# Kernel tuning notes

Hardware: AMD Instinct MI355X
Metric: run time of the kernel (lower is better)

## Reference

```python
import jax, jax.numpy as jnp
import numpy as np

N_NODES = 100000
N_EDGES = 1600000
D_FEAT = 128
HIDDEN = 128
N_CLASSES = 10
N_GRAPHS = 64


def setup_inputs() -> dict:
    key = jax.random.key(0)
    ks = jax.random.split(key, 8)
    x = jax.random.normal(ks[0], (N_NODES, D_FEAT), dtype=jnp.float32)
    edge_index = jax.random.randint(ks[1], (2, N_EDGES), 0, N_NODES, dtype=jnp.int64)
    batch = jnp.sort(jax.random.randint(ks[2], (N_NODES,), 0, N_GRAPHS, dtype=jnp.int64))
    # GraphConv params: lin_rel (weight+bias) applied to aggregated neighbors,
    # lin_root (weight only) applied to self features. Final classifier lin.
    s = 1.0 / np.sqrt(D_FEAT)
    w_rel = jax.random.uniform(ks[3], (HIDDEN, D_FEAT), jnp.float32, -s, s)
    b_rel = jax.random.uniform(ks[4], (HIDDEN,), jnp.float32, -s, s)
    w_root = jax.random.uniform(ks[5], (HIDDEN, D_FEAT), jnp.float32, -s, s)
    sl = 1.0 / np.sqrt(HIDDEN)
    w_lin = jax.random.uniform(ks[6], (N_CLASSES, HIDDEN), jnp.float32, -sl, sl)
    b_lin = jax.random.uniform(ks[7], (N_CLASSES,), jnp.float32, -sl, sl)
    return {"x": x, "edge_index": edge_index, "batch": batch,
            "w_rel": w_rel, "b_rel": b_rel, "w_root": w_root,
            "w_lin": w_lin, "b_lin": b_lin}


def reference(x, edge_index, batch, w_rel, b_rel, w_root, w_lin, b_lin):
    src, dst = edge_index[0], edge_index[1]
    # GraphConv(aggr='add'): gather source features, scatter-add to targets
    agg = jax.ops.segment_sum(x[src], dst, num_segments=N_NODES)  # [N, F]
    h = agg @ w_rel.T + b_rel + x @ w_root.T                      # [N, H]
    # global_mean_pool over graph ids
    summed = jax.ops.segment_sum(h, batch, num_segments=N_GRAPHS)            # [G, H]
    counts = jax.ops.segment_sum(jnp.ones((N_NODES,), h.dtype), batch,
                                 num_segments=N_GRAPHS)                       # [G]
    pooled = summed / jnp.maximum(counts, 1.0)[:, None]
    # final classifier (dropout==0 so it is a no-op)
    return pooled @ w_lin.T + b_lin                                # [G, C]
```

## Files before the change

kernel.cpp:

```cpp
#include <hip/hip_runtime.h>

#define N_NODES  100000
#define N_EDGES  1600000
#define D        128
#define NG       64
#define NC       10
#define NBMAX    512
#define TILE     64
#define EPT      8
#define ABLK     196
#define NBUCK    391
#define BCAP     8192
#define CBLK2    98
#define CIW      68
#define XSW      130

typedef unsigned int uint;
typedef unsigned short ushort;
typedef unsigned long long ull;
typedef short bhalf8 __attribute__((ext_vector_type(8)));
typedef float f32x4  __attribute__((ext_vector_type(4)));

#define MFMA_BF16 __builtin_amdgcn_mfma_f32_16x16x32_bf16

#define OFF_COUNTS 391
#define ZERO_U32   512
#define BDATA_U32  (NBUCK * (BCAP / 2))

static_assert(ABLK * 1024 * EPT >= N_EDGES, "edge coverage");
static_assert(NBUCK * 256 >= N_NODES, "bucket coverage");

__global__ __launch_bounds__(256) void fill_kernel(uint* __restrict__ p)
{
    const int i = blockIdx.x * 256 + threadIdx.x;
    if (i < ZERO_U32) p[i] = 0u;
}

__global__ __launch_bounds__(1024) void bucket_kernel(
    const int* __restrict__ ei, const int* __restrict__ batch,
    uint* __restrict__ tail, int* __restrict__ counts,
    ushort* __restrict__ bdata)
{
    const int b = blockIdx.x;
    if (b < ABLK) {
        __shared__ uint hs[NBUCK];
        __shared__ uint he[NBUCK];
        const int t = threadIdx.x;
        for (int i = t; i < NBUCK; i += 1024) hs[i] = 0u;
        __syncthreads();

        const int e0 = b * (1024 * EPT) + t * EPT;
        uint er[EPT];
        int  s[EPT], dn[EPT];
        bool v[EPT];
        if (e0 + EPT <= N_EDGES) {
            const int4 a0 = *reinterpret_cast<const int4*>(ei + e0);
            const int4 a1 = *reinterpret_cast<const int4*>(ei + e0 + 4);
            const int4 b0 = *reinterpret_cast<const int4*>(ei + N_EDGES + e0);
            const int4 b1 = *reinterpret_cast<const int4*>(ei + N_EDGES + e0 + 4);
            s[0]=a0.x; s[1]=a0.y; s[2]=a0.z; s[3]=a0.w;
            s[4]=a1.x; s[5]=a1.y; s[6]=a1.z; s[7]=a1.w;
            dn[0]=b0.x; dn[1]=b0.y; dn[2]=b0.z; dn[3]=b0.w;
            dn[4]=b1.x; dn[5]=b1.y; dn[6]=b1.z; dn[7]=b1.w;
            #pragma unroll
            for (int i = 0; i < EPT; ++i) v[i] = true;
        } else {
            #pragma unroll
            for (int i = 0; i < EPT; ++i) {
                v[i] = (e0 + i) < N_EDGES;
                s[i]  = v[i] ? ei[e0 + i] : 0;
                dn[i] = v[i] ? ei[N_EDGES + e0 + i] : 0;
            }
        }
        #pragma unroll
        for (int i = 0; i < EPT; ++i) {
            if (v[i]) {
                const uint g = (uint)batch[dn[i]];
                const uint k = (uint)s[i] >> 8;
                er[i] = (k << 16) | (((uint)s[i] & 255u) << 6) | g;
                atomicAdd(&hs[k], 1u);
            } else er[i] = 0xFFFFFFFFu;
        }
        __syncthreads();
        if (t < NBUCK) {
            const uint c = hs[t];
            uint r = 0u, a = 0u;
            if (c) { a = (c + 31u) & ~31u; r = atomicAdd(&tail[t], a); }
            hs[t] = r;
            he[t] = r + a;
        }
        __syncthreads();
        #pragma unroll
        for (int i = 0; i < EPT; ++i) {
            if (er[i] != 0xFFFFFFFFu) {
                const uint k = er[i] >> 16;
                const uint pos = atomicAdd(&hs[k], 1u);
                if (pos < BCAP)
                    bdata[(size_t)k * BCAP + pos] = (ushort)(er[i] & 0xFFFFu);
            }
        }
        __syncthreads();
        if (t < NBUCK) {
            uint p = hs[t];
            uint e = he[t];
            if (e > BCAP) e = BCAP;
            for (; p < e; ++p) bdata[(size_t)t * BCAP + p] = 0xFFFFu;
        }
    } else {
        const int n = (b - ABLK) * 1024 + threadIdx.x;
        if (n >= N_NODES) return;
        const int lane = threadIdx.x & 63;
        const int g = batch[n];
        const bool lead = (n == 0) || (lane == 0) || (batch[n - 1] != g);
        const ull bl = __ballot(lead);
        if (lead) {
            const ull higher = (lane == 63) ? 0ull : (bl >> (lane + 1));
            int end = higher ? (lane + 1 + (__ffsll(higher) - 1)) : 64;
            const int wb = n - lane;
            int nv = N_NODES - wb; if (nv > 64) nv = 64;
            if (end > nv) end = nv;
            atomicAdd(&counts[g], end - lane);
        }
    }
}

__device__ __forceinline__ uint packbf(float f)
{
    const uint u  = __float_as_uint(f);
    const uint hb = (u + 0x7FFFu + ((u >> 16) & 1u)) >> 16;
    const float hf = __uint_as_float(hb << 16);
    const uint ul = __float_as_uint(f - hf);
    const uint lb = (ul + 0x7FFFu + ((ul >> 16) & 1u)) >> 16;
    return hb | (lb << 16);
}

__global__ __launch_bounds__(1024, 8) void gemm_kernel(
    const float* __restrict__ x,
    const uint* __restrict__ tail, const ushort* __restrict__ bdata,
    const int* __restrict__ batch,
    float* __restrict__ partA, float* __restrict__ partX, int NBe)
{
    __shared__ uint xsp[TILE * XSW];
    __shared__ uint ci[NG * CIW];
    __shared__ uint h[TILE * NG];

    const int t   = threadIdx.x;
    const int l   = t & 63;
    const int w   = t >> 6;
    const int mt  = w & 3;
    const int nt0 = (w >> 2) << 1;
    const int lr  = l & 15;
    const int lh  = l >> 4;

    f32x4 aA0 = {0,0,0,0}, aA1 = {0,0,0,0};
    f32x4 aX0 = {0,0,0,0}, aX1 = {0,0,0,0};

    const int ntiles = (N_NODES + TILE - 1) / TILE;
    for (int tb = blockIdx.x; tb < ntiles; tb += NBe) {
        const int base   = tb * TILE;
        const int nvalid = min(TILE, N_NODES - base);
        const int bk     = tb >> 2;
        const uint qsel  = (uint)(tb & 3);

        #pragma unroll
        for (int k = 0; k < 4; ++k) h[t + k * 1024] = 0u;
        #pragma unroll
        for (int k = 0; k < 2; ++k) {
            const int f4i = t + k * 1024;
            const int n = f4i >> 5, c4 = f4i & 31;
            float4 v = make_float4(0.f, 0.f, 0.f, 0.f);
            if (n < nvalid)
                v = *reinterpret_cast<const float4*>(x + (size_t)(base + n) * D + c4 * 4);
            uint2 p01, p23;
            p01.x = packbf(v.x); p01.y = packbf(v.y);
            p23.x = packbf(v.z); p23.y = packbf(v.w);
            uint* dst = xsp + n * XSW + c4 * 4;
            *reinterpret_cast<uint2*>(dst)     = p01;
            *reinterpret_cast<uint2*>(dst + 2) = p23;
        }
        __syncthreads();

        {
            uint nrec = tail[bk]; if (nrec > BCAP) nrec = BCAP;
            const ushort* __restrict__ bp = bdata + (size_t)bk * BCAP;
            for (uint i = (uint)t; i < nrec; i += 1024u) {
                const uint r = bp[i];
                if (r != 0xFFFFu && ((r >> 12) & 3u) == qsel)
                    atomicAdd(&h[((r >> 6) & 63u) * NG + (r & 63u)], 1u);
            }
        }
        __syncthreads();

        {
            const int node = t >> 4, slot = t & 15;
            const int gb = (node < nvalid) ? batch[base + node] : -1;
            const uint4 hv = *reinterpret_cast<const uint4*>(&h[node * NG + slot * 4]);
            const uint hc[4] = {hv.x, hv.y, hv.z, hv.w};
            #pragma unroll
            for (int j = 0; j < 4; ++j) {
                const int g = slot * 4 + j;
                uint val = __float_as_uint((float)hc[j]) >> 16;
                if (gb == g) val |= 0x3F800000u;
                ci[g * CIW + node] = val;
            }
        }
        __syncthreads();

        #pragma unroll
        for (int kc = 0; kc < 2; ++kc) {
            const int k0 = kc * 32;
            const uint* cip = ci + (mt * 16 + lr) * CIW + k0 + lh * 8;
            const uint4 ca = *reinterpret_cast<const uint4*>(cip);
            const uint4 cb = *reinterpret_cast<const uint4*>(cip + 4);
            bhalf8 acnt, aind;
            acnt[0]=(short)ca.x; aind[0]=(short)(ca.x>>16);
            acnt[1]=(short)ca.y; aind[1]=(short)(ca.y>>16);
            acnt[2]=(short)ca.z; aind[2]=(short)(ca.z>>16);
            acnt[3]=(short)ca.w; aind[3]=(short)(ca.w>>16);
            acnt[4]=(short)cb.x; aind[4]=(short)(cb.x>>16);
            acnt[5]=(short)cb.y; aind[5]=(short)(cb.y>>16);
            acnt[6]=(short)cb.z; aind[6]=(short)(cb.z>>16);
            acnt[7]=(short)cb.w; aind[7]=(short)(cb.w>>16);

            const uint* xb = xsp + (k0 + lh * 8) * XSW + lr;
            {
                const uint* xp = xb + nt0 * 16;
                const uint r0=xp[0],      r1=xp[XSW],   r2=xp[2*XSW], r3=xp[3*XSW],
                           r4=xp[4*XSW],  r5=xp[5*XSW], r6=xp[6*XSW], r7=xp[7*XSW];
                bhalf8 bh, bl;
                bh[0]=(short)r0; bl[0]=(short)(r0>>16);
                bh[1]=(short)r1; bl[1]=(short)(r1>>16);
                bh[2]=(short)r2; bl[2]=(short)(r2>>16);
                bh[3]=(short)r3; bl[3]=(short)(r3>>16);
                bh[4]=(short)r4; bl[4]=(short)(r4>>16);
                bh[5]=(short)r5; bl[5]=(short)(r5>>16);
                bh[6]=(short)r6; bl[6]=(short)(r6>>16);
                bh[7]=(short)r7; bl[7]=(short)(r7>>16);
                aA0 = MFMA_BF16(acnt, bh, aA0, 0, 0, 0);
                aA0 = MFMA_BF16(acnt, bl, aA0, 0, 0, 0);
                aX0 = MFMA_BF16(aind, bh, aX0, 0, 0, 0);
                aX0 = MFMA_BF16(aind, bl, aX0, 0, 0, 0);
            }
            {
                const uint* xp = xb + (nt0 + 1) * 16;
                const uint r0=xp[0],      r1=xp[XSW],   r2=xp[2*XSW], r3=xp[3*XSW],
                           r4=xp[4*XSW],  r5=xp[5*XSW], r6=xp[6*XSW], r7=xp[7*XSW];
                bhalf8 bh, bl;
                bh[0]=(short)r0; bl[0]=(short)(r0>>16);
                bh[1]=(short)r1; bl[1]=(short)(r1>>16);
                bh[2]=(short)r2; bl[2]=(short)(r2>>16);
                bh[3]=(short)r3; bl[3]=(short)(r3>>16);
                bh[4]=(short)r4; bl[4]=(short)(r4>>16);
                bh[5]=(short)r5; bl[5]=(short)(r5>>16);
                bh[6]=(short)r6; bl[6]=(short)(r6>>16);
                bh[7]=(short)r7; bl[7]=(short)(r7>>16);
                aA1 = MFMA_BF16(acnt, bh, aA1, 0, 0, 0);
                aA1 = MFMA_BF16(acnt, bl, aA1, 0, 0, 0);
                aX1 = MFMA_BF16(aind, bh, aX1, 0, 0, 0);
                aX1 = MFMA_BF16(aind, bl, aX1, 0, 0, 0);
            }
        }
        __syncthreads();
    }

    float* pa = partA + (size_t)blockIdx.x * (NG * D);
    float* px = partX + (size_t)blockIdx.x * (NG * D);
    #pragma unroll
    for (int r = 0; r < 4; ++r) {
        const int row = mt * 16 + lh * 4 + r;
        pa[row * D + nt0 * 16 + lr]       = aA0[r];
        pa[row * D + (nt0 + 1) * 16 + lr] = aA1[r];
        px[row * D + nt0 * 16 + lr]       = aX0[r];
        px[row * D + (nt0 + 1) * 16 + lr] = aX1[r];
    }
}

__global__ __launch_bounds__(256) void reduce1_kernel(
    const float* __restrict__ partA, const float* __restrict__ partX,
    float* __restrict__ tmp2, int NBe)
{
    const int cb = blockIdx.x & 63;
    const int pc = blockIdx.x >> 6;
    const int c  = cb * 256 + threadIdx.x;
    const float* __restrict__ srcp =
        (c < NG * D) ? (partA + c) : (partX + (c - NG * D));
    const int chunk = (NBe + 3) >> 2;
    const int p0 = pc * chunk;
    int p1 = p0 + chunk; if (p1 > NBe) p1 = NBe;
    float s = 0.f;
    #pragma unroll 8
    for (int p = p0; p < p1; ++p) s += srcp[(size_t)p * (NG * D)];
    tmp2[pc * (2 * NG * D) + c] = s;
}

__global__ __launch_bounds__(128) void final_kernel(
    const float* __restrict__ tmp2, const int* __restrict__ counts,
    const float* __restrict__ w_rel, const float* __restrict__ b_rel,
    const float* __restrict__ w_root,
    const float* __restrict__ w_lin, const float* __restrict__ b_lin,
    float* __restrict__ out)
{
    const int g = blockIdx.x;
    const int t = threadIdx.x;

    __shared__ float agg_s[D], x_s[D], p_s[D];
    float a = 0.f, xsum = 0.f;
    #pragma unroll
    for (int j = 0; j < 4; ++j) {
        a    += tmp2[j * (2 * NG * D) + g * D + t];
        xsum += tmp2[j * (2 * NG * D) + NG * D + g * D + t];
    }
    agg_s[t] = a; x_s[t] = xsum;
    __syncthreads();

    const float cn = (float)counts[g];
    float hj = b_rel[t] * cn;
    const float* __restrict__ wr = w_rel  + (size_t)t * D;
    const float* __restrict__ wo = w_root + (size_t)t * D;
    #pragma unroll 8
    for (int d0 = 0; d0 < D; ++d0) hj += agg_s[d0] * wr[d0] + x_s[d0] * wo[d0];
    p_s[t] = hj / fmaxf(cn, 1.f);
    __syncthreads();

    if (t < NC) {
        const float* __restrict__ wl = w_lin + (size_t)t * D;
        float o = b_lin[t];
        #pragma unroll 8
        for (int d0 = 0; d0 < D; ++d0) o += p_s[d0] * wl[d0];
        out[g * NC + t] = o;
    }
}

extern "C" void kernel_launch(void* const* d_in, const int* in_sizes, int n_in,
                              void* d_out, int out_size, void* d_ws, size_t ws_size,
                              hipStream_t stream)
{
    const float* x      = (const float*)d_in[0];
    const int*   ei     = (const int*)  d_in[1];
    const int*   batch  = (const int*)  d_in[2];
    const float* w_rel  = (const float*)d_in[3];
    const float* b_rel  = (const float*)d_in[4];
    const float* w_root = (const float*)d_in[5];
    const float* w_lin  = (const float*)d_in[6];
    const float* b_lin  = (const float*)d_in[7];
    float* out = (float*)d_out;

    uint*   tail   = (uint*)d_ws;
    int*    counts = (int*)(tail + OFF_COUNTS);
    ushort* bdata  = (ushort*)(tail + ZERO_U32);
    float*  partA  = (float*)(tail + ZERO_U32 + BDATA_U32);

    const size_t availf = ws_size / sizeof(float);
    const size_t headf  = ZERO_U32 + BDATA_U32;
    const size_t tmp2f  = 4 * (size_t)(2 * NG * D);
    int NBe = NBMAX;
    if (headf + tmp2f + (size_t)NBe * 2 * NG * D > availf) {
        long long rem = (long long)availf - (long long)(headf + tmp2f);
        long long nb  = rem / (2 * NG * D);
        NBe = (nb < 1) ? 1 : (int)nb;
    }
    float* partX = partA + (size_t)NBe * NG * D;
    float* tmp2  = partX + (size_t)NBe * NG * D;

    fill_kernel<<<2, 256, 0, stream>>>(tail);
    bucket_kernel<<<ABLK + CBLK2, 1024, 0, stream>>>(ei, batch, tail, counts, bdata);
    gemm_kernel<<<NBe, 1024, 0, stream>>>(x, tail, bdata, batch, partA, partX, NBe);
    reduce1_kernel<<<256, 256, 0, stream>>>(partA, partX, tmp2, NBe);
    final_kernel<<<NG, 128, 0, stream>>>(tmp2, counts,
                                         w_rel, b_rel, w_root, w_lin, b_lin, out);
}
```

Before: 78.92 us.

## Move per-graph x sums into bucket kernel via atomics, halving gemm MFMA work

The per-graph sum of x (the root term) was computed inside the gemm kernel using an indicator matrix and extra MFMAs, then written to partial buffers and reduced. It is now computed in the bucket kernel's node blocks, which run-length accumulate consecutive nodes of the same graph and add the result to a small global buffer with float atomics. The gemm kernel therefore issues half the MFMAs, writes half the partials and builds a 16-bit count matrix loaded directly as a bf16 vector, and the reduce kernel reads half as much data. In exchange the bucket kernel re-reads all of x, which adds memory traffic, and the float atomics make the result order-dependent.

```diff
diff --git a/kernel.cpp b/kernel.cpp
--- a/kernel.cpp
+++ b/kernel.cpp
@@ -11,8 +11,8 @@
 #define ABLK     196
 #define NBUCK    391
 #define BCAP     8192
-#define CBLK2    98
-#define CIW      68
+#define XBLK     196
+#define CIW16    72
 #define XSW      130
 
 typedef unsigned int uint;
@@ -24,11 +24,13 @@
 #define MFMA_BF16 __builtin_amdgcn_mfma_f32_16x16x32_bf16
 
 #define OFF_COUNTS 391
-#define ZERO_U32   512
+#define OFF_AGGX   512
+#define ZERO_U32   8704
 #define BDATA_U32  (NBUCK * (BCAP / 2))
 
 static_assert(ABLK * 1024 * EPT >= N_EDGES, "edge coverage");
 static_assert(NBUCK * 256 >= N_NODES, "bucket coverage");
+static_assert(XBLK * 512 >= N_NODES, "node coverage");
 
 __global__ __launch_bounds__(256) void fill_kernel(uint* __restrict__ p)
 {
@@ -38,8 +40,9 @@
 
 __global__ __launch_bounds__(1024) void bucket_kernel(
     const int* __restrict__ ei, const int* __restrict__ batch,
+    const float* __restrict__ x,
     uint* __restrict__ tail, int* __restrict__ counts,
-    ushort* __restrict__ bdata)
+    float* __restrict__ aggX, ushort* __restrict__ bdata)
 {
     const int b = blockIdx.x;
     if (b < ABLK) {
@@ -107,19 +110,51 @@
             for (; p < e; ++p) bdata[(size_t)t * BCAP + p] = 0xFFFFu;
         }
     } else {
-        const int n = (b - ABLK) * 1024 + threadIdx.x;
-        if (n >= N_NODES) return;
-        const int lane = threadIdx.x & 63;
-        const int g = batch[n];
-        const bool lead = (n == 0) || (lane == 0) || (batch[n - 1] != g);
-        const ull bl = __ballot(lead);
-        if (lead) {
-            const ull higher = (lane == 63) ? 0ull : (bl >> (lane + 1));
-            int end = higher ? (lane + 1 + (__ffsll(higher) - 1)) : 64;
-            const int wb = n - lane;
-            int nv = N_NODES - wb; if (nv > 64) nv = 64;
-            if (end > nv) end = nv;
-            atomicAdd(&counts[g], end - lane);
+        const int nb = b - ABLK;
+        const int t  = threadIdx.x;
+
+        if (t < 512) {
+            const int n = nb * 512 + t;
+            if (n < N_NODES) {
+                const int lane = t & 63;
+                const int g = batch[n];
+                const bool lead = (n == 0) || (lane == 0) || (batch[n - 1] != g);
+                const ull bl = __ballot(lead);
+                if (lead) {
+                    const ull higher = (lane == 63) ? 0ull : (bl >> (lane + 1));
+                    int end = higher ? (lane + 1 + (__ffsll(higher) - 1)) : 64;
+                    const int wb = n - lane;
+                    int nv = N_NODES - wb; if (nv > 64) nv = 64;
+                    if (end > nv) end = nv;
+                    atomicAdd(&counts[g], end - lane);
+                }
+            }
+        }
+
+        {
+            const int w16 = t >> 6, l = t & 63;
+            const int n0 = nb * 512 + w16 * 32;
+            float2 rs = {0.f, 0.f};
+            int cg = -1;
+            for (int i = 0; i < 32; ++i) {
+                const int n = n0 + i;
+                if (n >= N_NODES) break;
+                const int g = batch[n];
+                const float2 v =
+                    *reinterpret_cast<const float2*>(x + (size_t)n * D + 2 * l);
+                if (g != cg) {
+                    if (cg >= 0) {
+                        unsafeAtomicAdd(&aggX[cg * D + 2 * l],     rs.x);
+                        unsafeAtomicAdd(&aggX[cg * D + 2 * l + 1], rs.y);
+                    }
+                    rs.x = 0.f; rs.y = 0.f; cg = g;
+                }
+                rs.x += v.x; rs.y += v.y;
+            }
+            if (cg >= 0) {
+                unsafeAtomicAdd(&aggX[cg * D + 2 * l],     rs.x);
+                unsafeAtomicAdd(&aggX[cg * D + 2 * l + 1], rs.y);
+            }
         }
     }
 }
@@ -137,12 +172,11 @@
 __global__ __launch_bounds__(1024, 8) void gemm_kernel(
     const float* __restrict__ x,
     const uint* __restrict__ tail, const ushort* __restrict__ bdata,
-    const int* __restrict__ batch,
-    float* __restrict__ partA, float* __restrict__ partX, int NBe)
-{
-    __shared__ uint xsp[TILE * XSW];
-    __shared__ uint ci[NG * CIW];
-    __shared__ uint h[TILE * NG];
+    float* __restrict__ partA, int NBe)
+{
+    __shared__ uint   xsp[TILE * XSW];
+    __shared__ ushort ci16[NG * CIW16];
+    __shared__ uint   h[TILE * NG];
 
     const int t   = threadIdx.x;
     const int l   = t & 63;
@@ -153,7 +187,6 @@
     const int lh  = l >> 4;
 
     f32x4 aA0 = {0,0,0,0}, aA1 = {0,0,0,0};
-    f32x4 aX0 = {0,0,0,0}, aX1 = {0,0,0,0};
 
     const int ntiles = (N_NODES + TILE - 1) / TILE;
     for (int tb = blockIdx.x; tb < ntiles; tb += NBe) {
@@ -192,35 +225,24 @@
         __syncthreads();
 
         {
-            const int node = t >> 4, slot = t & 15;
-            const int gb = (node < nvalid) ? batch[base + node] : -1;
-            const uint4 hv = *reinterpret_cast<const uint4*>(&h[node * NG + slot * 4]);
-            const uint hc[4] = {hv.x, hv.y, hv.z, hv.w};
-            #pragma unroll
-            for (int j = 0; j < 4; ++j) {
-                const int g = slot * 4 + j;
-                uint val = __float_as_uint((float)hc[j]) >> 16;
-                if (gb == g) val |= 0x3F800000u;
-                ci[g * CIW + node] = val;
-            }
+            const int g  = t & 63;
+            const int n4 = (t >> 6) * 4;
+            ushort c0 = (ushort)(__float_as_uint((float)h[(n4 + 0) * NG + g]) >> 16);
+            ushort c1 = (ushort)(__float_as_uint((float)h[(n4 + 1) * NG + g]) >> 16);
+            ushort c2 = (ushort)(__float_as_uint((float)h[(n4 + 2) * NG + g]) >> 16);
+            ushort c3 = (ushort)(__float_as_uint((float)h[(n4 + 3) * NG + g]) >> 16);
+            uint2 pk;
+            pk.x = (uint)c0 | ((uint)c1 << 16);
+            pk.y = (uint)c2 | ((uint)c3 << 16);
+            *reinterpret_cast<uint2*>(&ci16[g * CIW16 + n4]) = pk;
         }
         __syncthreads();
 
         #pragma unroll
         for (int kc = 0; kc < 2; ++kc) {
             const int k0 = kc * 32;
-            const uint* cip = ci + (mt * 16 + lr) * CIW + k0 + lh * 8;
-            const uint4 ca = *reinterpret_cast<const uint4*>(cip);
-            const uint4 cb = *reinterpret_cast<const uint4*>(cip + 4);
-            bhalf8 acnt, aind;
-            acnt[0]=(short)ca.x; aind[0]=(short)(ca.x>>16);
-            acnt[1]=(short)ca.y; aind[1]=(short)(ca.y>>16);
-            acnt[2]=(short)ca.z; aind[2]=(short)(ca.z>>16);
-            acnt[3]=(short)ca.w; aind[3]=(short)(ca.w>>16);
-            acnt[4]=(short)cb.x; aind[4]=(short)(cb.x>>16);
-            acnt[5]=(short)cb.y; aind[5]=(short)(cb.y>>16);
-            acnt[6]=(short)cb.z; aind[6]=(short)(cb.z>>16);
-            acnt[7]=(short)cb.w; aind[7]=(short)(cb.w>>16);
+            const bhalf8 acnt = *reinterpret_cast<const bhalf8*>(
+                &ci16[(mt * 16 + lr) * CIW16 + k0 + lh * 8]);
 
             const uint* xb = xsp + (k0 + lh * 8) * XSW + lr;
             {
@@ -238,8 +260,6 @@
                 bh[7]=(short)r7; bl[7]=(short)(r7>>16);
                 aA0 = MFMA_BF16(acnt, bh, aA0, 0, 0, 0);
                 aA0 = MFMA_BF16(acnt, bl, aA0, 0, 0, 0);
-                aX0 = MFMA_BF16(aind, bh, aX0, 0, 0, 0);
-                aX0 = MFMA_BF16(aind, bl, aX0, 0, 0, 0);
             }
             {
                 const uint* xp = xb + (nt0 + 1) * 16;
@@ -256,45 +276,38 @@
                 bh[7]=(short)r7; bl[7]=(short)(r7>>16);
                 aA1 = MFMA_BF16(acnt, bh, aA1, 0, 0, 0);
                 aA1 = MFMA_BF16(acnt, bl, aA1, 0, 0, 0);
-                aX1 = MFMA_BF16(aind, bh, aX1, 0, 0, 0);
-                aX1 = MFMA_BF16(aind, bl, aX1, 0, 0, 0);
             }
         }
         __syncthreads();
     }
 
     float* pa = partA + (size_t)blockIdx.x * (NG * D);
-    float* px = partX + (size_t)blockIdx.x * (NG * D);
     #pragma unroll
     for (int r = 0; r < 4; ++r) {
         const int row = mt * 16 + lh * 4 + r;
         pa[row * D + nt0 * 16 + lr]       = aA0[r];
         pa[row * D + (nt0 + 1) * 16 + lr] = aA1[r];
-        px[row * D + nt0 * 16 + lr]       = aX0[r];
-        px[row * D + (nt0 + 1) * 16 + lr] = aX1[r];
     }
 }
 
 __global__ __launch_bounds__(256) void reduce1_kernel(
-    const float* __restrict__ partA, const float* __restrict__ partX,
-    float* __restrict__ tmp2, int NBe)
-{
-    const int cb = blockIdx.x & 63;
-    const int pc = blockIdx.x >> 6;
+    const float* __restrict__ partA, float* __restrict__ tmp2, int NBe)
+{
+    const int cb = blockIdx.x & 31;
+    const int pc = blockIdx.x >> 5;
     const int c  = cb * 256 + threadIdx.x;
-    const float* __restrict__ srcp =
-        (c < NG * D) ? (partA + c) : (partX + (c - NG * D));
     const int chunk = (NBe + 3) >> 2;
     const int p0 = pc * chunk;
     int p1 = p0 + chunk; if (p1 > NBe) p1 = NBe;
     float s = 0.f;
     #pragma unroll 8
-    for (int p = p0; p < p1; ++p) s += srcp[(size_t)p * (NG * D)];
-    tmp2[pc * (2 * NG * D) + c] = s;
+    for (int p = p0; p < p1; ++p) s += partA[(size_t)p * (NG * D) + c];
+    tmp2[pc * (NG * D) + c] = s;
 }
 
 __global__ __launch_bounds__(128) void final_kernel(
-    const float* __restrict__ tmp2, const int* __restrict__ counts,
+    const float* __restrict__ tmp2, const float* __restrict__ aggX,
+    const int* __restrict__ counts,
     const float* __restrict__ w_rel, const float* __restrict__ b_rel,
     const float* __restrict__ w_root,
     const float* __restrict__ w_lin, const float* __restrict__ b_lin,
@@ -304,13 +317,11 @@
     const int t = threadIdx.x;
 
     __shared__ float agg_s[D], x_s[D], p_s[D];
-    float a = 0.f, xsum = 0.f;
+    float a = 0.f;
     #pragma unroll
-    for (int j = 0; j < 4; ++j) {
-        a    += tmp2[j * (2 * NG * D) + g * D + t];
-        xsum += tmp2[j * (2 * NG * D) + NG * D + g * D + t];
-    }
-    agg_s[t] = a; x_s[t] = xsum;
+    for (int j = 0; j < 4; ++j) a += tmp2[j * (NG * D) + g * D + t];
+    agg_s[t] = a;
+    x_s[t]   = aggX[(size_t)g * D + t];
     __syncthreads();
 
     const float cn = (float)counts[g];
@@ -347,25 +358,26 @@
 
     uint*   tail   = (uint*)d_ws;
     int*    counts = (int*)(tail + OFF_COUNTS);
+    float*  aggX   = (float*)(tail + OFF_AGGX);
     ushort* bdata  = (ushort*)(tail + ZERO_U32);
     float*  partA  = (float*)(tail + ZERO_U32 + BDATA_U32);
 
     const size_t availf = ws_size / sizeof(float);
     const size_t headf  = ZERO_U32 + BDATA_U32;
-    const size_t tmp2f  = 4 * (size_t)(2 * NG * D);
+    const size_t tmp2f  = 4 * (size_t)(NG * D);
     int NBe = NBMAX;
-    if (headf + tmp2f + (size_t)NBe * 2 * NG * D > availf) {
+    if (headf + tmp2f + (size_t)NBe * NG * D > availf) {
         long long rem = (long long)availf - (long long)(headf + tmp2f);
-        long long nb  = rem / (2 * NG * D);
+        long long nb  = rem / (NG * D);
         NBe = (nb < 1) ? 1 : (int)nb;
     }
-    float* partX = partA + (size_t)NBe * NG * D;
-    float* tmp2  = partX + (size_t)NBe * NG * D;
-
-    fill_kernel<<<2, 256, 0, stream>>>(tail);
-    bucket_kernel<<<ABLK + CBLK2, 1024, 0, stream>>>(ei, batch, tail, counts, bdata);
-    gemm_kernel<<<NBe, 1024, 0, stream>>>(x, tail, bdata, batch, partA, partX, NBe);
-    reduce1_kernel<<<256, 256, 0, stream>>>(partA, partX, tmp2, NBe);
-    final_kernel<<<NG, 128, 0, stream>>>(tmp2, counts,
+    float* tmp2 = partA + (size_t)NBe * NG * D;
+
+    fill_kernel<<<(ZERO_U32 + 255) / 256, 256, 0, stream>>>(tail);
+    bucket_kernel<<<ABLK + XBLK, 1024, 0, stream>>>(ei, batch, x, tail, counts,
+                                                    aggX, bdata);
+    gemm_kernel<<<NBe, 1024, 0, stream>>>(x, tail, bdata, partA, NBe);
+    reduce1_kernel<<<128, 256, 0, stream>>>(partA, tmp2, NBe);
+    final_kernel<<<NG, 128, 0, stream>>>(tmp2, aggX, counts,
                                          w_rel, b_rel, w_root, w_lin, b_lin, out);
 }
```

Result: slower. 85.10 us (+7.8%).
